# Performance work log

Measured on AMD Instinct MI355X. Metric: run time of the kernel, lower is better.

The kernel has to match this reference:

```python
import jax, jax.numpy as jnp
import numpy as np

T, H, NLAYER = 16, 1024, 4  # timesteps, hidden (== broadcast batch), layers


def setup_inputs() -> dict:
    key = jax.random.key(0)
    ks = jax.random.split(key, 18)
    f = lambda k, s: 0.05 * jax.random.normal(k, s, dtype=jnp.float32)
    inp = {"x": jax.random.normal(ks[0], (T, H, 1), dtype=jnp.float32)}
    # input->gate weights, shape (in_dim=1, H) per layer, stacked over layers
    inp["Wxi"] = f(ks[1], (NLAYER, 1, H))
    inp["Wxf"] = f(ks[2], (NLAYER, 1, H))
    inp["Wxc"] = f(ks[3], (NLAYER, 1, H))
    inp["Wxo"] = f(ks[4], (NLAYER, 1, H))
    # recurrent weights (H, H) per layer
    inp["Whi"] = f(ks[5], (NLAYER, H, H))
    inp["Whf"] = f(ks[6], (NLAYER, H, H))
    inp["Whc"] = f(ks[7], (NLAYER, H, H))
    inp["Who"] = f(ks[8], (NLAYER, H, H))
    # layer-skip weights (applied to h of layer below), layers 1..NLAYER-1
    inp["Whsi"] = f(ks[9], (NLAYER - 1, H, H))
    inp["Whsf"] = f(ks[10], (NLAYER - 1, H, H))
    inp["Whsc"] = f(ks[11], (NLAYER - 1, H, H))
    inp["Whso"] = f(ks[12], (NLAYER - 1, H, H))
    # biases (1, H) per layer
    inp["bi"] = f(ks[13], (NLAYER, 1, H))
    inp["bf"] = f(ks[14], (NLAYER, 1, H))
    inp["bc"] = f(ks[15], (NLAYER, 1, H))
    inp["bo"] = f(ks[16], (NLAYER, 1, H))
    return inp


def reference(x, Wxi, Wxf, Wxc, Wxo, Whi, Whf, Whc, Who,
              Whsi, Whsf, Whsc, Whso, bi, bf, bc, bo):
    nlayer, hs = Whi.shape[0], Whi.shape[1]
    c0 = jnp.zeros((nlayer, hs, hs), x.dtype)
    h0 = jnp.zeros((nlayer, hs, hs), x.dtype)

    def step(carry, xt):
        c_1, h_1 = carry  # each (nlayer, H, H); xt: (H, 1)
        cs, hs_ = [], []
        for i in range(nlayer):
            si = hs_[i - 1] * Whsi[i - 1] if i > 0 else 0.0
            sf = hs_[i - 1] * Whsf[i - 1] if i > 0 else 0.0
            so = hs_[i - 1] * Whso[i - 1] if i > 0 else 0.0
            sc = hs_[i - 1] * Whsc[i - 1] if i > 0 else 0.0
            _i = jax.nn.sigmoid(xt * Wxi[i] + si + h_1[i] * Whi[i] + bi[i])
            _f = jax.nn.sigmoid(xt * Wxf[i] + sf + h_1[i] * Whf[i] + bf[i])
            _o = jax.nn.sigmoid(xt * Wxo[i] + so + h_1[i] * Who[i] + bo[i])
            _c = jnp.tanh(xt * Wxc[i] + sc + h_1[i] * Whc[i] + bc[i])
            c_new = _f * c_1[i] + _i * _c
            cs.append(c_new)
            hs_.append(_o * jnp.tanh(c_new))
        c = jnp.stack(cs)
        h = jnp.stack(hs_)
        return (c, h), jnp.stack([c, h])

    _, ys = jax.lax.scan(step, (c0, h0), x)
    return ys  # (T, 2, nlayer, H, H): stacked (c, h) per timestep, like tf.scan
```

## Files before the change

### kernel.cpp

```cpp
#include <hip/hip_runtime.h>


constexpr int T  = 16;
constexpr int H  = 1024;
constexpr int NL = 4;
constexpr int HH = H * H;

__device__ __forceinline__ float sigmoid_f(float z) {
    return __builtin_amdgcn_rcpf(1.0f + __expf(-z));
}
__device__ __forceinline__ float tanh_f(float z) {
    return fmaf(2.0f, sigmoid_f(2.0f * z), -1.0f);
}

__global__ __launch_bounds__(256)
void slstm_kernel(const float* __restrict__ x,
                  const float* __restrict__ Wxi, const float* __restrict__ Wxf,
                  const float* __restrict__ Wxc, const float* __restrict__ Wxo,
                  const float* __restrict__ Whi, const float* __restrict__ Whf,
                  const float* __restrict__ Whc, const float* __restrict__ Who,
                  const float* __restrict__ Whsi, const float* __restrict__ Whsf,
                  const float* __restrict__ Whsc, const float* __restrict__ Whso,
                  const float* __restrict__ bi, const float* __restrict__ bf,
                  const float* __restrict__ bc, const float* __restrict__ bo,
                  float* __restrict__ out)
{
    const int idx = blockIdx.x * blockDim.x + threadIdx.x;
    const int r = idx >> 10;
    const int c = idx & (H - 1);

    float whi[NL], whf[NL], whc[NL], who[NL];
    float wxi[NL], wxf[NL], wxc[NL], wxo[NL];
    float vbi[NL], vbf[NL], vbc[NL], vbo[NL];
#pragma unroll
    for (int i = 0; i < NL; ++i) {
        whi[i] = Whi[i * HH + idx];
        whf[i] = Whf[i * HH + idx];
        whc[i] = Whc[i * HH + idx];
        who[i] = Who[i * HH + idx];
        wxi[i] = Wxi[i * H + c];
        wxf[i] = Wxf[i * H + c];
        wxc[i] = Wxc[i * H + c];
        wxo[i] = Wxo[i * H + c];
        vbi[i] = bi[i * H + c];
        vbf[i] = bf[i * H + c];
        vbc[i] = bc[i * H + c];
        vbo[i] = bo[i * H + c];
    }
    float wsi[NL - 1], wsf[NL - 1], wsc[NL - 1], wso[NL - 1];
#pragma unroll
    for (int j = 0; j < NL - 1; ++j) {
        wsi[j] = Whsi[j * HH + idx];
        wsf[j] = Whsf[j * HH + idx];
        wsc[j] = Whsc[j * HH + idx];
        wso[j] = Whso[j * HH + idx];
    }

    float cs[NL] = {0.f, 0.f, 0.f, 0.f};
    float hs[NL] = {0.f, 0.f, 0.f, 0.f};

    for (int t = 0; t < T; ++t) {
        const float xv = x[t * H + r];
        float* outp = out + (size_t)t * (2 * NL * HH) + idx;
        float hbelow = 0.0f;
#pragma unroll
        for (int i = 0; i < NL; ++i) {
            float zi = fmaf(xv, wxi[i], fmaf(hs[i], whi[i], vbi[i]));
            float zf = fmaf(xv, wxf[i], fmaf(hs[i], whf[i], vbf[i]));
            float zc = fmaf(xv, wxc[i], fmaf(hs[i], whc[i], vbc[i]));
            float zo = fmaf(xv, wxo[i], fmaf(hs[i], who[i], vbo[i]));
            if (i > 0) {
                zi = fmaf(hbelow, wsi[i - 1], zi);
                zf = fmaf(hbelow, wsf[i - 1], zf);
                zc = fmaf(hbelow, wsc[i - 1], zc);
                zo = fmaf(hbelow, wso[i - 1], zo);
            }
            const float ig = sigmoid_f(zi);
            const float fg = sigmoid_f(zf);
            const float og = sigmoid_f(zo);
            const float cc = tanh_f(zc);
            const float cn = fmaf(fg, cs[i], ig * cc);
            const float hn = og * tanh_f(cn);
            cs[i] = cn;
            hs[i] = hn;
            hbelow = hn;
            outp[(size_t)i * HH]        = cn;
            outp[(size_t)(NL + i) * HH] = hn;
        }
    }
}

extern "C" void kernel_launch(void* const* d_in, const int* in_sizes, int n_in,
                              void* d_out, int out_size, void* d_ws, size_t ws_size,
                              hipStream_t stream) {
    const float* x    = (const float*)d_in[0];
    const float* Wxi  = (const float*)d_in[1];
    const float* Wxf  = (const float*)d_in[2];
    const float* Wxc  = (const float*)d_in[3];
    const float* Wxo  = (const float*)d_in[4];
    const float* Whi  = (const float*)d_in[5];
    const float* Whf  = (const float*)d_in[6];
    const float* Whc  = (const float*)d_in[7];
    const float* Who  = (const float*)d_in[8];
    const float* Whsi = (const float*)d_in[9];
    const float* Whsf = (const float*)d_in[10];
    const float* Whsc = (const float*)d_in[11];
    const float* Whso = (const float*)d_in[12];
    const float* bi   = (const float*)d_in[13];
    const float* bf   = (const float*)d_in[14];
    const float* bc   = (const float*)d_in[15];
    const float* bo   = (const float*)d_in[16];
    float* out = (float*)d_out;

    dim3 grid(HH / 256), block(256);
    slstm_kernel<<<grid, block, 0, stream>>>(x, Wxi, Wxf, Wxc, Wxo,
                                             Whi, Whf, Whc, Who,
                                             Whsi, Whsf, Whsc, Whso,
                                             bi, bf, bc, bo, out);
}
```

Baseline: 654.6 us.

## Prescale weights by log2e, use exp2, nontemporal loads/stores, prefetch x

Folds the log2(e) factors into the weights and biases at load time so each gate uses exp2 directly instead of exp, which saves a multiply per transcendental. It also switches the one-shot weight loads and all output stores to nontemporal hints, prefetches the next timestep's x value, and adds an occupancy hint of 4 to launch_bounds. The kernel writes a large output stream, so the store path is the main target. The prescaling adds a small rounding difference.

```diff
diff --git a/kernel.cpp b/kernel.cpp
--- a/kernel.cpp
+++ b/kernel.cpp
@@ -6,14 +6,24 @@
 constexpr int NL = 4;
 constexpr int HH = H * H;
 
-__device__ __forceinline__ float sigmoid_f(float z) {
-    return __builtin_amdgcn_rcpf(1.0f + __expf(-z));
+constexpr float L2E  = 1.4426950408889634f;
+constexpr float L2E2 = 2.8853900817779268f;
+
+__device__ __forceinline__ float exp2_fast(float x) {
+#if __has_builtin(__builtin_amdgcn_exp2f)
+    return __builtin_amdgcn_exp2f(x);
+#else
+    return __expf(x * 0.6931471805599453f);
+#endif
 }
-__device__ __forceinline__ float tanh_f(float z) {
-    return fmaf(2.0f, sigmoid_f(2.0f * z), -1.0f);
+__device__ __forceinline__ float sig_p(float z2) {
+    return __builtin_amdgcn_rcpf(1.0f + exp2_fast(-z2));
+}
+__device__ __forceinline__ float tanh_p(float z2) {
+    return fmaf(2.0f, __builtin_amdgcn_rcpf(1.0f + exp2_fast(-z2)), -1.0f);
 }
 
-__global__ __launch_bounds__(256)
+__global__ __launch_bounds__(256, 4)
 void slstm_kernel(const float* __restrict__ x,
                   const float* __restrict__ Wxi, const float* __restrict__ Wxf,
                   const float* __restrict__ Wxc, const float* __restrict__ Wxo,
@@ -34,34 +44,39 @@
     float vbi[NL], vbf[NL], vbc[NL], vbo[NL];
 #pragma unroll
     for (int i = 0; i < NL; ++i) {
-        whi[i] = Whi[i * HH + idx];
-        whf[i] = Whf[i * HH + idx];
-        whc[i] = Whc[i * HH + idx];
-        who[i] = Who[i * HH + idx];
-        wxi[i] = Wxi[i * H + c];
-        wxf[i] = Wxf[i * H + c];
-        wxc[i] = Wxc[i * H + c];
-        wxo[i] = Wxo[i * H + c];
-        vbi[i] = bi[i * H + c];
-        vbf[i] = bf[i * H + c];
-        vbc[i] = bc[i * H + c];
-        vbo[i] = bo[i * H + c];
+        whi[i] = __builtin_nontemporal_load(&Whi[i * HH + idx]) * L2E;
+        whf[i] = __builtin_nontemporal_load(&Whf[i * HH + idx]) * L2E;
+        whc[i] = __builtin_nontemporal_load(&Whc[i * HH + idx]) * L2E2;
+        who[i] = __builtin_nontemporal_load(&Who[i * HH + idx]) * L2E;
+        wxi[i] = Wxi[i * H + c] * L2E;
+        wxf[i] = Wxf[i * H + c] * L2E;
+        wxc[i] = Wxc[i * H + c] * L2E2;
+        wxo[i] = Wxo[i * H + c] * L2E;
+        vbi[i] = bi[i * H + c] * L2E;
+        vbf[i] = bf[i * H + c] * L2E;
+        vbc[i] = bc[i * H + c] * L2E2;
+        vbo[i] = bo[i * H + c] * L2E;
     }
     float wsi[NL - 1], wsf[NL - 1], wsc[NL - 1], wso[NL - 1];
 #pragma unroll
     for (int j = 0; j < NL - 1; ++j) {
-        wsi[j] = Whsi[j * HH + idx];
-        wsf[j] = Whsf[j * HH + idx];
-        wsc[j] = Whsc[j * HH + idx];
-        wso[j] = Whso[j * HH + idx];
+        wsi[j] = __builtin_nontemporal_load(&Whsi[j * HH + idx]) * L2E;
+        wsf[j] = __builtin_nontemporal_load(&Whsf[j * HH + idx]) * L2E;
+        wsc[j] = __builtin_nontemporal_load(&Whsc[j * HH + idx]) * L2E2;
+        wso[j] = __builtin_nontemporal_load(&Whso[j * HH + idx]) * L2E;
     }
 
     float cs[NL] = {0.f, 0.f, 0.f, 0.f};
     float hs[NL] = {0.f, 0.f, 0.f, 0.f};
 
+    float xv = x[r];
+    float* outp = out + idx;
+
     for (int t = 0; t < T; ++t) {
-        const float xv = x[t * H + r];
-        float* outp = out + (size_t)t * (2 * NL * HH) + idx;
+        const int tn = (t + 1) & (T - 1) ? (t + 1) : t;
+        const float xnext = x[(t + 1 < T ? t + 1 : t) * H + r];
+        (void)tn;
+
         float hbelow = 0.0f;
 #pragma unroll
         for (int i = 0; i < NL; ++i) {
@@ -75,18 +90,20 @@
                 zc = fmaf(hbelow, wsc[i - 1], zc);
                 zo = fmaf(hbelow, wso[i - 1], zo);
             }
-            const float ig = sigmoid_f(zi);
-            const float fg = sigmoid_f(zf);
-            const float og = sigmoid_f(zo);
-            const float cc = tanh_f(zc);
+            const float ig = sig_p(zi);
+            const float fg = sig_p(zf);
+            const float og = sig_p(zo);
+            const float cc = tanh_p(zc);
             const float cn = fmaf(fg, cs[i], ig * cc);
-            const float hn = og * tanh_f(cn);
+            const float hn = og * tanh_p(cn * L2E2);
             cs[i] = cn;
             hs[i] = hn;
             hbelow = hn;
-            outp[(size_t)i * HH]        = cn;
-            outp[(size_t)(NL + i) * HH] = hn;
+            __builtin_nontemporal_store(cn, outp + (size_t)i * HH);
+            __builtin_nontemporal_store(hn, outp + (size_t)(NL + i) * HH);
         }
+        xv = xnext;
+        outp += (size_t)(2 * NL) * HH;
     }
 }
 
```

New measurement: 637.5 us. 2.6% less time.
